# Optimization experiments

Hardware: AMD Instinct MI355X
Metric: run time of the kernel (lower is better)

## Reference

```python
import jax, jax.numpy as jnp
import numpy as np

B, N, K, D = 4096, 64, 48, 64   # batch, n_features, n_bins, d_embedding
F = N * D                        # flattened embedding dim
E, H, O = 8, 1024, 512           # experts, expert hidden, expert out
T, TH = 2, 256                   # tasks, tower hidden


def setup_inputs() -> dict:
    key = jax.random.key(0)
    ks = jax.random.split(key, 10)
    # PLE buffers from uniform bins linspace(0,1,K+1): w = 1/width, b = -edge/width
    edges = jnp.linspace(0.0, 1.0, K + 1)
    width = jnp.diff(edges)
    w = 1.0 / width                      # (K,)
    b = -edges[:-1] / width              # (K,)
    ple_weight = jnp.broadcast_to(w, (N, K)).astype(jnp.float32)
    ple_bias = jnp.broadcast_to(b, (N, K)).astype(jnp.float32)
    s = lambda fan_in: fan_in ** -0.5
    return {
        "x": jax.random.uniform(ks[0], (B, N), jnp.float32),
        "ple_weight": ple_weight,
        "ple_bias": ple_bias,
        "emb_W": jax.random.normal(ks[1], (N, K, D), jnp.float32) * s(K),
        "emb_b": jax.random.normal(ks[2], (N, D), jnp.float32) * s(K),
        "gate_W": jax.random.normal(ks[3], (F, E), jnp.float32) * s(F),
        "gate_b": jnp.zeros((E,), jnp.float32),
        "e_W1": jax.random.normal(ks[4], (E, F, H), jnp.float32) * s(F),
        "e_b1": jnp.zeros((E, H), jnp.float32),
        "e_W2": jax.random.normal(ks[5], (E, H, O), jnp.float32) * s(H),
        "e_b2": jnp.zeros((E, O), jnp.float32),
        "tw1": jax.random.normal(ks[6], (T, O, TH), jnp.float32) * s(O),
        "tb1": jnp.zeros((T, TH), jnp.float32),
        "tw2": jax.random.normal(ks[7], (T, TH, 1), jnp.float32) * s(TH),
        "tb2": jnp.zeros((T, 1), jnp.float32),
        "top_k": 2,
    }


def reference(x, ple_weight, ple_bias, emb_W, emb_b, gate_W, gate_b,
              e_W1, e_b1, e_W2, e_b2, tw1, tb1, tw2, tb2, top_k):
    # --- Piecewise Linear Encoding: (B, N) -> (B, N, K) ---
    enc = ple_bias + ple_weight * x[..., None]
    enc = jnp.concatenate([
        jnp.minimum(enc[..., :1], 1.0),
        jnp.clip(enc[..., 1:-1], 0.0, 1.0),
        jnp.maximum(enc[..., -1:], 0.0),
    ], axis=-1)
    # --- PLE embeddings via NLinear + ReLU: (B, N, K) -> (B, N, D) ---
    emb = jax.nn.relu(jnp.einsum("bnk,nkd->bnd", enc, emb_W) + emb_b)
    flat = emb.reshape(emb.shape[0], -1)                 # (B, F)
    # --- Sparse MoE gating (softmax + top-k renormalized) ---
    probs = jax.nn.softmax(flat @ gate_W + gate_b, axis=-1)   # (B, E)
    topv, topi = jax.lax.top_k(probs, top_k)
    topv = topv / jnp.sum(topv, axis=-1, keepdims=True)
    gates = jnp.zeros_like(probs).at[jnp.arange(probs.shape[0])[:, None], topi].set(topv)
    # --- Experts (computed densely, gated combine) ---
    h = jax.nn.relu(jnp.einsum("bf,efh->beh", flat, e_W1) + e_b1)   # (B, E, H)
    eo = jnp.einsum("beh,eho->beo", h, e_W2) + e_b2                 # (B, E, O)
    moe = jnp.einsum("be,beo->bo", gates, eo)                       # (B, O)
    # --- Task towers: per-task MLP -> scalar ---
    th = jax.nn.relu(jnp.einsum("bo,tos->bts", moe, tw1) + tb1)     # (B, T, TH)
    out = (jnp.einsum("bts,tsu->btu", th, tw2) + tb2)[..., 0]       # (B, T)
    return out
```

## Files before the change

kernel.cpp:

```cpp
#include <hip/hip_runtime.h>
#include <cstdint>

#define B_ 4096
#define N_ 64
#define K_ 48
#define D_ 64
#define F_ 4096
#define E_ 8
#define H_ 1024
#define O_ 512
#define T_ 2
#define TH_ 256
#define NSLOT (B_ * 2)

#define MAXT1 72

typedef float f32x4 __attribute__((ext_vector_type(4)));
typedef __bf16 bf16x8 __attribute__((ext_vector_type(8)));

__device__ __forceinline__ unsigned short f2bf(float f) {
    union { float f; unsigned int u; } v; v.f = f;
    unsigned int u = v.u;
    u += 0x7FFFu + ((u >> 16) & 1u);
    return (unsigned short)(u >> 16);
}

__device__ __forceinline__ void gload_lds16(const void* gptr, void* lptr) {
    auto* g = reinterpret_cast<const __attribute__((address_space(1))) unsigned int*>(
        reinterpret_cast<uintptr_t>(gptr));
    auto* l = reinterpret_cast<__attribute__((address_space(3))) unsigned int*>(
        reinterpret_cast<uintptr_t>(lptr));
    __builtin_amdgcn_global_load_lds(g, l, 16, 0, 0);
}

__global__ __launch_bounds__(64) void prefix_kernel(
    const float* __restrict__ embW, const float* __restrict__ embB,
    float* __restrict__ P)
{
    int n = blockIdx.x;
    int lane = threadIdx.x;
    float acc = embB[n * D_ + lane];
    const float* wsrc = embW + (size_t)n * K_ * D_ + lane;
    float* dst = P + (size_t)n * K_ * D_ + lane;
    #pragma unroll 8
    for (int k = 0; k < K_; ++k) {
        dst[k * D_] = acc;
        acc += wsrc[k * D_];
    }
}

__global__ __launch_bounds__(256) void ple_embed_kernel(
    const float* __restrict__ x, const float* __restrict__ plw,
    const float* __restrict__ plb, const float* __restrict__ embW,
    const float* __restrict__ P, const float* __restrict__ gateW,
    unsigned short* __restrict__ flat_bf, float* __restrict__ logits)
{
    __shared__ float gpart[4][E_];
    int b = blockIdx.x;
    int tid = threadIdx.x, lane = tid & 63, w = tid >> 6;

    float xl = x[b * N_ + lane];
    float gp[E_];
    #pragma unroll
    for (int e = 0; e < E_; ++e) gp[e] = 0.0f;

    #pragma unroll 4
    for (int i = 0; i < 16; ++i) {
        int n = w * 16 + i;
        float xn = __shfl(xl, n);
        const float* pw = plw + n * K_;
        const float* pb = plb + n * K_;
        float t = fmaf(pw[0], xn, pb[0]);
        int j = (int)t;
        j = max(0, min(K_ - 1, j));
        float f = fminf(fmaxf(fmaf(pw[j], xn, pb[j]), 0.0f), 1.0f);
        size_t base = ((size_t)n * K_ + j) * D_ + lane;
        float emb = fmaxf(fmaf(f, embW[base], P[base]), 0.0f);
        flat_bf[(size_t)b * F_ + n * D_ + lane] = f2bf(emb);

        const float4* gw4 = (const float4*)(gateW + (size_t)(n * D_ + lane) * E_);
        float4 g0 = gw4[0], g1 = gw4[1];
        gp[0] = fmaf(emb, g0.x, gp[0]);
        gp[1] = fmaf(emb, g0.y, gp[1]);
        gp[2] = fmaf(emb, g0.z, gp[2]);
        gp[3] = fmaf(emb, g0.w, gp[3]);
        gp[4] = fmaf(emb, g1.x, gp[4]);
        gp[5] = fmaf(emb, g1.y, gp[5]);
        gp[6] = fmaf(emb, g1.z, gp[6]);
        gp[7] = fmaf(emb, g1.w, gp[7]);
    }

    #pragma unroll
    for (int off = 32; off > 0; off >>= 1) {
        #pragma unroll
        for (int e = 0; e < E_; ++e) gp[e] += __shfl_down(gp[e], off);
    }
    if (lane == 0) {
        #pragma unroll
        for (int e = 0; e < E_; ++e) gpart[w][e] = gp[e];
    }
    __syncthreads();
    if (tid < E_)
        logits[b * E_ + tid] =
            gpart[0][tid] + gpart[1][tid] + gpart[2][tid] + gpart[3][tid];
}

__global__ __launch_bounds__(256) void gate_top2_kernel(
    const float* __restrict__ logits, const float* __restrict__ gate_b,
    int* __restrict__ topi, float* __restrict__ topg, int* __restrict__ counts)
{
    int b = blockIdx.x * 256 + threadIdx.x;
    int lane = threadIdx.x & 63;
    float l[E_];
    #pragma unroll
    for (int e = 0; e < E_; ++e) l[e] = logits[b * E_ + e] + gate_b[e];
    int e1 = 0; float v1 = l[0];
    #pragma unroll
    for (int e = 1; e < E_; ++e) if (l[e] > v1) { v1 = l[e]; e1 = e; }
    int e2 = -1; float v2 = -1e30f;
    #pragma unroll
    for (int e = 0; e < E_; ++e) if (e != e1 && l[e] > v2) { v2 = l[e]; e2 = e; }
    float ex = expf(v2 - v1);
    float g1 = 1.0f / (1.0f + ex);
    float g2 = ex / (1.0f + ex);
    topi[b * 2] = e1; topi[b * 2 + 1] = e2;
    topg[b * 2] = g1; topg[b * 2 + 1] = g2;
    #pragma unroll
    for (int e = 0; e < E_; ++e) {
        unsigned long long m1 = __ballot(e1 == e);
        unsigned long long m2 = __ballot(e2 == e);
        if (lane == 0) {
            int c = __popcll(m1) + __popcll(m2);
            if (c) atomicAdd(&counts[e], c);
        }
    }
}

__global__ void scan_kernel(const int* __restrict__ counts, int* __restrict__ offsets,
                            int* __restrict__ tiles1, int* __restrict__ ntiles) {
    int e = threadIdx.x;
    if (e >= E_) return;
    int c[E_];
    #pragma unroll
    for (int i = 0; i < E_; ++i) c[i] = counts[i];
    int off = 0, tb = 0, tot = 0, ttot = 0;
    #pragma unroll
    for (int i = 0; i < E_; ++i) {
        int t = (c[i] + 127) >> 7;
        if (i < e) { off += c[i]; tb += t; }
        tot += c[i]; ttot += t;
    }
    offsets[e] = off;
    if (e == 0) { offsets[E_] = tot; ntiles[0] = ttot; }
    int nt = (c[e] + 127) >> 7;
    for (int tr = 0; tr < nt; ++tr) tiles1[tb + tr] = (e << 16) | tr;
}

__global__ __launch_bounds__(256) void scatter_kernel(
    const int* __restrict__ topi, const float* __restrict__ topg,
    const int* __restrict__ offsets, int* __restrict__ cursors,
    int* __restrict__ rows, float* __restrict__ gatev)
{
    int b = blockIdx.x * 256 + threadIdx.x;
    int lane = threadIdx.x & 63;
    #pragma unroll
    for (int j = 0; j < 2; ++j) {
        int e = topi[b * 2 + j];
        float g = topg[b * 2 + j];
        #pragma unroll
        for (int ex = 0; ex < E_; ++ex) {
            unsigned long long m = __ballot(e == ex);
            if (e == ex) {
                int leader = __builtin_ctzll(m);
                int base = 0;
                if (lane == leader) base = atomicAdd(&cursors[ex], __popcll(m));
                base = __shfl(base, leader);
                int pos = base + __popcll(m & ((1ull << lane) - 1ull));
                int slot = offsets[ex] + pos;
                rows[slot] = b;
                gatev[slot] = g;
            }
        }
    }
}

__global__ __launch_bounds__(256) void transp_bf16_kernel(
    const float* __restrict__ in, unsigned short* __restrict__ out, int R, int C)
{
    __shared__ float tile[64][65];
    int ch = blockIdx.z;
    const float* src = in + (size_t)ch * R * C;
    unsigned short* dst = out + (size_t)ch * R * C;
    int c0 = blockIdx.x * 64, r0 = blockIdx.y * 64;
    int lane = threadIdx.x & 63, w = threadIdx.x >> 6;
    #pragma unroll
    for (int i = 0; i < 16; ++i) {
        int r = w * 16 + i;
        tile[r][lane] = src[(size_t)(r0 + r) * C + c0 + lane];
    }
    __syncthreads();
    #pragma unroll
    for (int i = 0; i < 16; ++i) {
        int c = w * 16 + i;
        dst[(size_t)(c0 + c) * R + r0 + lane] = f2bf(tile[lane][c]);
    }
}

__global__ __launch_bounds__(256) void fc1_kernel(
    const unsigned short* __restrict__ Abf,
    const unsigned short* __restrict__ Wbt,
    const float* __restrict__ bias,
    const int* __restrict__ rows, const int* __restrict__ offsets,
    const int* __restrict__ tiles1, const int* __restrict__ ntiles,
    unsigned short* __restrict__ Hbf)
{
    int bid = blockIdx.x;
    int tile = bid >> 3, cn = bid & 7;
    if (tile >= ntiles[0]) return;
    int te = tiles1[tile];
    int e = te >> 16, tr = te & 0xffff;
    int m0 = offsets[e], mEnd = offsets[e + 1];
    int Me = mEnd - m0;

    __shared__ alignas(16) unsigned short As[128 * 64];
    __shared__ alignas(16) unsigned short Bs[128 * 64];

    int tid = threadIdx.x, lane = tid & 63, wv = tid >> 6;
    int lr = lane >> 3;
    int pchunk = lane & 7;
    int cg = pchunk ^ lr;

    const unsigned short* aptr[4];
    const unsigned short* bptr[4];
    #pragma unroll
    for (int i = 0; i < 4; ++i) {
        int reg = wv * 4 + i;
        int rowA = reg * 8 + lr;
        int slot = min(m0 + tr * 128 + rowA, mEnd - 1);
        aptr[i] = Abf + (size_t)rows[slot] * F_ + cg * 8;
        int rowB = cn * 128 + reg * 8 + lr;
        bptr[i] = Wbt + ((size_t)e * H_ + rowB) * (size_t)F_ + cg * 8;
    }

    f32x4 zero = {0.f, 0.f, 0.f, 0.f};
    f32x4 acc[4][4];
    #pragma unroll
    for (int i = 0; i < 4; ++i)
        #pragma unroll
        for (int j = 0; j < 4; ++j) acc[i][j] = zero;

    int wvM = wv >> 1, wvN = wv & 1;
    int m16 = lane & 15, q = lane >> 4;

    for (int k0 = 0; k0 < F_; k0 += 64) {
        __syncthreads();
        #pragma unroll
        for (int i = 0; i < 4; ++i) {
            int reg = wv * 4 + i;
            gload_lds16(aptr[i] + k0, &As[reg * 512]);
            gload_lds16(bptr[i] + k0, &Bs[reg * 512]);
        }
        __syncthreads();
        #pragma unroll
        for (int ks = 0; ks < 2; ++ks) {
            bf16x8 af[4], bfg[4];
            #pragma unroll
            for (int mt = 0; mt < 4; ++mt) {
                int m = wvM * 64 + mt * 16 + m16;
                int pos = (ks * 4 + q) ^ (m & 7);
                af[mt] = *(const bf16x8*)&As[m * 64 + pos * 8];
            }
            #pragma unroll
            for (int nt = 0; nt < 4; ++nt) {
                int n = wvN * 64 + nt * 16 + m16;
                int pos = (ks * 4 + q) ^ (n & 7);
                bfg[nt] = *(const bf16x8*)&Bs[n * 64 + pos * 8];
            }
            #pragma unroll
            for (int mt = 0; mt < 4; ++mt)
                #pragma unroll
                for (int nt = 0; nt < 4; ++nt)
                    acc[mt][nt] = __builtin_amdgcn_mfma_f32_16x16x32_bf16(
                        af[mt], bfg[nt], acc[mt][nt], 0, 0, 0);
        }
    }

    #pragma unroll
    for (int nt = 0; nt < 4; ++nt) {
        int col = cn * 128 + wvN * 64 + nt * 16 + m16;
        float bv = bias[e * H_ + col];
        #pragma unroll
        for (int mt = 0; mt < 4; ++mt) {
            int rbase = tr * 128 + wvM * 64 + mt * 16 + q * 4;
            #pragma unroll
            for (int r = 0; r < 4; ++r) {
                int rr = rbase + r;
                if (rr < Me) {
                    float v = fmaxf(acc[mt][nt][r] + bv, 0.0f);
                    Hbf[(size_t)(m0 + rr) * H_ + col] = f2bf(v);
                }
            }
        }
    }
}

__global__ __launch_bounds__(256) void fc2_kernel(
    const unsigned short* __restrict__ Hbf,
    const unsigned short* __restrict__ Wbt,
    const float* __restrict__ bias,
    const int* __restrict__ rows, const float* __restrict__ gatev,
    const int* __restrict__ offsets, const int* __restrict__ tiles1,
    const int* __restrict__ ntiles, float* __restrict__ moe)
{
    int bid = blockIdx.x;
    int tile = bid >> 3, cn = bid & 7;
    if (tile >= ntiles[0]) return;
    int te = tiles1[tile];
    int e = te >> 16, tr = te & 0xffff;
    int m0 = offsets[e], mEnd = offsets[e + 1];
    int Me = mEnd - m0;

    __shared__ alignas(16) unsigned short As[128 * 64];
    __shared__ alignas(16) unsigned short Bs[64 * 64];

    int tid = threadIdx.x, lane = tid & 63, wv = tid >> 6;
    int lr = lane >> 3;
    int pchunk = lane & 7;
    int cg = pchunk ^ lr;

    const unsigned short* aptr[4];
    const unsigned short* bptr[2];
    #pragma unroll
    for (int i = 0; i < 4; ++i) {
        int rowA = (wv * 4 + i) * 8 + lr;
        int slot = min(m0 + tr * 128 + rowA, mEnd - 1);
        aptr[i] = Hbf + (size_t)slot * H_ + cg * 8;
    }
    #pragma unroll
    for (int i = 0; i < 2; ++i) {
        int rowB = cn * 64 + (wv * 2 + i) * 8 + lr;
        bptr[i] = Wbt + ((size_t)e * O_ + rowB) * (size_t)H_ + cg * 8;
    }

    f32x4 zero = {0.f, 0.f, 0.f, 0.f};
    f32x4 acc[4][2];
    #pragma unroll
    for (int i = 0; i < 4; ++i)
        #pragma unroll
        for (int j = 0; j < 2; ++j) acc[i][j] = zero;

    int wvM = wv >> 1, wvN = wv & 1;
    int m16 = lane & 15, q = lane >> 4;

    for (int k0 = 0; k0 < H_; k0 += 64) {
        __syncthreads();
        #pragma unroll
        for (int i = 0; i < 4; ++i)
            gload_lds16(aptr[i] + k0, &As[(wv * 4 + i) * 512]);
        #pragma unroll
        for (int i = 0; i < 2; ++i)
            gload_lds16(bptr[i] + k0, &Bs[(wv * 2 + i) * 512]);
        __syncthreads();
        #pragma unroll
        for (int ks = 0; ks < 2; ++ks) {
            bf16x8 af[4], bfg[2];
            #pragma unroll
            for (int mt = 0; mt < 4; ++mt) {
                int m = wvM * 64 + mt * 16 + m16;
                int pos = (ks * 4 + q) ^ (m & 7);
                af[mt] = *(const bf16x8*)&As[m * 64 + pos * 8];
            }
            #pragma unroll
            for (int nt = 0; nt < 2; ++nt) {
                int n = wvN * 32 + nt * 16 + m16;
                int pos = (ks * 4 + q) ^ (n & 7);
                bfg[nt] = *(const bf16x8*)&Bs[n * 64 + pos * 8];
            }
            #pragma unroll
            for (int mt = 0; mt < 4; ++mt)
                #pragma unroll
                for (int nt = 0; nt < 2; ++nt)
                    acc[mt][nt] = __builtin_amdgcn_mfma_f32_16x16x32_bf16(
                        af[mt], bfg[nt], acc[mt][nt], 0, 0, 0);
        }
    }

    #pragma unroll
    for (int nt = 0; nt < 2; ++nt) {
        int col = cn * 64 + wvN * 32 + nt * 16 + m16;
        float bv = bias[e * O_ + col];
        #pragma unroll
        for (int mt = 0; mt < 4; ++mt) {
            int rbase = tr * 128 + wvM * 64 + mt * 16 + q * 4;
            #pragma unroll
            for (int r = 0; r < 4; ++r) {
                int rr = rbase + r;
                if (rr < Me) {
                    int slot = m0 + rr;
                    float g = gatev[slot];
                    int b = rows[slot];
                    atomicAdd(&moe[(size_t)b * O_ + col], g * (acc[mt][nt][r] + bv));
                }
            }
        }
    }
}

__global__ __launch_bounds__(256) void tower_kernel(
    const float* __restrict__ moe, const float* __restrict__ tw1,
    const float* __restrict__ tb1, const float* __restrict__ tw2,
    const float* __restrict__ tb2, float* __restrict__ out)
{
    __shared__ float ms[8 * O_];
    __shared__ float red[16][4];
    int b0 = blockIdx.x * 8;
    int tid = threadIdx.x, lane = tid & 63, wv = tid >> 6;
    for (int idx = tid; idx < 8 * O_; idx += 256)
        ms[idx] = moe[(size_t)b0 * O_ + idx];
    __syncthreads();

    int s = tid;
    float a0[8], a1[8];
    float bv0 = tb1[s], bv1 = tb1[TH_ + s];
    #pragma unroll
    for (int i = 0; i < 8; ++i) { a0[i] = bv0; a1[i] = bv1; }

    for (int o = 0; o < O_; o += 4) {
        float w0[4], w1[4];
        #pragma unroll
        for (int u = 0; u < 4; ++u) {
            w0[u] = tw1[(size_t)(o + u) * TH_ + s];
            w1[u] = tw1[(size_t)(O_ + o + u) * TH_ + s];
        }
        #pragma unroll
        for (int i = 0; i < 8; ++i) {
            float4 mv = *(const float4*)&ms[i * O_ + o];
            a0[i] = fmaf(mv.x, w0[0], a0[i]);
            a0[i] = fmaf(mv.y, w0[1], a0[i]);
            a0[i] = fmaf(mv.z, w0[2], a0[i]);
            a0[i] = fmaf(mv.w, w0[3], a0[i]);
            a1[i] = fmaf(mv.x, w1[0], a1[i]);
            a1[i] = fmaf(mv.y, w1[1], a1[i]);
            a1[i] = fmaf(mv.z, w1[2], a1[i]);
            a1[i] = fmaf(mv.w, w1[3], a1[i]);
        }
    }

    float w2a = tw2[s], w2b = tw2[TH_ + s];
    #pragma unroll
    for (int i = 0; i < 8; ++i) {
        float p0 = fmaxf(a0[i], 0.0f) * w2a;
        float p1 = fmaxf(a1[i], 0.0f) * w2b;
        #pragma unroll
        for (int off = 32; off > 0; off >>= 1) {
            p0 += __shfl_down(p0, off);
            p1 += __shfl_down(p1, off);
        }
        if (lane == 0) { red[i * 2 + 0][wv] = p0; red[i * 2 + 1][wv] = p1; }
    }
    __syncthreads();
    if (tid < 16) {
        int i = tid >> 1, t = tid & 1;
        float v = red[tid][0] + red[tid][1] + red[tid][2] + red[tid][3] + tb2[t];
        out[(size_t)(b0 + i) * T_ + t] = v;
    }
}

extern "C" void kernel_launch(void* const* d_in, const int* in_sizes, int n_in,
                              void* d_out, int out_size, void* d_ws, size_t ws_size,
                              hipStream_t stream)
{
    const float* x     = (const float*)d_in[0];
    const float* plw   = (const float*)d_in[1];
    const float* plb   = (const float*)d_in[2];
    const float* embW  = (const float*)d_in[3];
    const float* embB  = (const float*)d_in[4];
    const float* gateW = (const float*)d_in[5];
    const float* gateB = (const float*)d_in[6];
    const float* eW1   = (const float*)d_in[7];
    const float* eB1   = (const float*)d_in[8];
    const float* eW2   = (const float*)d_in[9];
    const float* eB2   = (const float*)d_in[10];
    const float* tw1   = (const float*)d_in[11];
    const float* tb1   = (const float*)d_in[12];
    const float* tw2   = (const float*)d_in[13];
    const float* tb2   = (const float*)d_in[14];
    float* out = (float*)d_out;

    char* w = (char*)d_ws;
    auto alloc = [&](size_t bytes) {
        char* p = w; w += (bytes + 255) & ~(size_t)255; return p;
    };
    unsigned short* flat_bf = (unsigned short*)alloc((size_t)B_ * F_ * 2);
    unsigned short* W1bt    = (unsigned short*)alloc((size_t)E_ * H_ * F_ * 2);
    unsigned short* W2bt    = (unsigned short*)alloc((size_t)E_ * O_ * H_ * 2);
    unsigned short* Hbf     = (unsigned short*)alloc((size_t)NSLOT * H_ * 2);
    float* Ppre    = (float*)alloc((size_t)N_ * K_ * D_ * 4);
    float* logits  = (float*)alloc((size_t)B_ * E_ * 4);
    float* moe     = (float*)alloc((size_t)B_ * O_ * 4);
    int*   topi    = (int*)alloc((size_t)B_ * 2 * 4);
    float* topg    = (float*)alloc((size_t)B_ * 2 * 4);
    int*   rows    = (int*)alloc((size_t)NSLOT * 4);
    float* gatev   = (float*)alloc((size_t)NSLOT * 4);
    int*   counts  = (int*)alloc(E_ * 4);
    int*   offsets = (int*)alloc((E_ + 1) * 4);
    int*   cursors = (int*)alloc(E_ * 4);
    int*   tiles1  = (int*)alloc(MAXT1 * 4);
    int*   ntiles  = (int*)alloc(2 * 4);

    hipMemsetAsync(moe, 0, (size_t)B_ * O_ * 4, stream);
    hipMemsetAsync(counts, 0, E_ * 4, stream);
    hipMemsetAsync(cursors, 0, E_ * 4, stream);

    prefix_kernel<<<N_, 64, 0, stream>>>(embW, embB, Ppre);
    ple_embed_kernel<<<B_, 256, 0, stream>>>(x, plw, plb, embW, Ppre, gateW,
                                             flat_bf, logits);
    transp_bf16_kernel<<<dim3(H_ / 64, F_ / 64, E_), 256, 0, stream>>>(eW1, W1bt, F_, H_);
    transp_bf16_kernel<<<dim3(O_ / 64, H_ / 64, E_), 256, 0, stream>>>(eW2, W2bt, H_, O_);
    gate_top2_kernel<<<B_ / 256, 256, 0, stream>>>(logits, gateB, topi, topg, counts);
    scan_kernel<<<1, 64, 0, stream>>>(counts, offsets, tiles1, ntiles);
    scatter_kernel<<<B_ / 256, 256, 0, stream>>>(topi, topg, offsets, cursors, rows, gatev);
    fc1_kernel<<<MAXT1 * 8, 256, 0, stream>>>(flat_bf, W1bt, eB1, rows, offsets,
                                              tiles1, ntiles, Hbf);
    fc2_kernel<<<MAXT1 * 8, 256, 0, stream>>>(Hbf, W2bt, eB2, rows, gatev, offsets,
                                              tiles1, ntiles, moe);
    tower_kernel<<<B_ / 8, 256, 0, stream>>>(moe, tw1, tb1, tw2, tb2, out);
}
```

Before: 574.8 us.

## Pre-swizzle expert weights into MFMA fragment layout and load B directly to registers

The weight conversion kernel now writes bf16 expert weights in a per-16x32 MFMA fragment order, so each lane can load its B operand with one contiguous 16-byte global read. Staging B through LDS is dropped in fc1 and fc2. fc1 tiles shrink from 128 to 64 columns with twice as many blocks, which raises parallelism but re-reads each A tile across 16 column blocks. B loads now go straight from global memory into registers with no LDS reuse across waves, so each wave's B fetch latency sits exposed inside the k-loop.

```diff
diff --git a/kernel.cpp b/kernel.cpp
--- a/kernel.cpp
+++ b/kernel.cpp
@@ -184,35 +184,145 @@
     }
 }
 
-__global__ __launch_bounds__(256) void transp_bf16_kernel(
+__global__ __launch_bounds__(256) void wfrag_kernel(
     const float* __restrict__ in, unsigned short* __restrict__ out, int R, int C)
 {
     __shared__ float tile[64][65];
-    int ch = blockIdx.z;
-    const float* src = in + (size_t)ch * R * C;
-    unsigned short* dst = out + (size_t)ch * R * C;
-    int c0 = blockIdx.x * 64, r0 = blockIdx.y * 64;
+    int e = blockIdx.z;
+    int rb = blockIdx.x, cb = blockIdx.y;
+    const float* src = in + (size_t)e * R * C + (size_t)(rb * 64) * C + cb * 64;
     int lane = threadIdx.x & 63, w = threadIdx.x >> 6;
     #pragma unroll
     for (int i = 0; i < 16; ++i) {
         int r = w * 16 + i;
-        tile[r][lane] = src[(size_t)(r0 + r) * C + c0 + lane];
+        tile[r][lane] = src[(size_t)r * C + lane];
     }
     __syncthreads();
-    #pragma unroll
-    for (int i = 0; i < 16; ++i) {
-        int c = w * 16 + i;
-        dst[(size_t)(c0 + c) * R + r0 + lane] = f2bf(tile[lane][c]);
+    int NB = C >> 4, KB = R >> 5;
+    #pragma unroll
+    for (int it = 0; it < 2; ++it) {
+        int t = threadIdx.x + it * 256;
+        int n0r = t >> 7, k0r = (t >> 6) & 1, ln = t & 63;
+        int q = ln >> 4, nl = ln & 15;
+        unsigned short v[8];
+        #pragma unroll
+        for (int j = 0; j < 8; ++j)
+            v[j] = f2bf(tile[k0r * 32 + q * 8 + j][n0r * 16 + nl]);
+        size_t didx = (((size_t)e * NB + cb * 4 + n0r) * KB + rb * 2 + k0r) * 512
+                      + (size_t)ln * 8;
+        uint4 pk;
+        pk.x = v[0] | ((unsigned)v[1] << 16);
+        pk.y = v[2] | ((unsigned)v[3] << 16);
+        pk.z = v[4] | ((unsigned)v[5] << 16);
+        pk.w = v[6] | ((unsigned)v[7] << 16);
+        *(uint4*)&out[didx] = pk;
     }
 }
 
 __global__ __launch_bounds__(256) void fc1_kernel(
     const unsigned short* __restrict__ Abf,
-    const unsigned short* __restrict__ Wbt,
+    const unsigned short* __restrict__ Wf,
     const float* __restrict__ bias,
     const int* __restrict__ rows, const int* __restrict__ offsets,
     const int* __restrict__ tiles1, const int* __restrict__ ntiles,
     unsigned short* __restrict__ Hbf)
+{
+    int bid = blockIdx.x;
+    int tile = bid >> 4, cn = bid & 15;
+    if (tile >= ntiles[0]) return;
+    int te = tiles1[tile];
+    int e = te >> 16, tr = te & 0xffff;
+    int m0 = offsets[e], mEnd = offsets[e + 1];
+    int Me = mEnd - m0;
+
+    __shared__ alignas(16) unsigned short As[128 * 64];
+
+    int tid = threadIdx.x, lane = tid & 63, wv = tid >> 6;
+    int lr = lane >> 3;
+    int cg = (lane & 7) ^ lr;
+
+    const unsigned short* aptr[4];
+    #pragma unroll
+    for (int i = 0; i < 4; ++i) {
+        int rowA = (wv * 4 + i) * 8 + lr;
+        int slot = min(m0 + tr * 128 + rowA, mEnd - 1);
+        aptr[i] = Abf + (size_t)rows[slot] * F_ + cg * 8;
+    }
+
+    int wvM = wv >> 1, wvN = wv & 1;
+    int m16 = lane & 15, q = lane >> 4;
+
+    const unsigned short* bbase[2];
+    #pragma unroll
+    for (int nt = 0; nt < 2; ++nt) {
+        int n0 = cn * 4 + wvN * 2 + nt;
+        bbase[nt] = Wf + (((size_t)e * (H_ / 16) + n0) * (F_ / 32)) * 512
+                    + (size_t)lane * 8;
+    }
+
+    f32x4 zero = {0.f, 0.f, 0.f, 0.f};
+    f32x4 acc[4][2];
+    #pragma unroll
+    for (int i = 0; i < 4; ++i)
+        #pragma unroll
+        for (int j = 0; j < 2; ++j) acc[i][j] = zero;
+
+    for (int k0 = 0; k0 < F_; k0 += 64) {
+        __syncthreads();
+        #pragma unroll
+        for (int i = 0; i < 4; ++i)
+            gload_lds16(aptr[i] + k0, &As[(wv * 4 + i) * 512]);
+        bf16x8 bfr[2][2];
+        #pragma unroll
+        for (int nt = 0; nt < 2; ++nt)
+            #pragma unroll
+            for (int ks = 0; ks < 2; ++ks)
+                bfr[nt][ks] = *(const bf16x8*)(bbase[nt] + (size_t)k0 * 16 + ks * 512);
+        __syncthreads();
+        #pragma unroll
+        for (int ks = 0; ks < 2; ++ks) {
+            bf16x8 af[4];
+            #pragma unroll
+            for (int mt = 0; mt < 4; ++mt) {
+                int m = wvM * 64 + mt * 16 + m16;
+                int pos = (ks * 4 + q) ^ (m & 7);
+                af[mt] = *(const bf16x8*)&As[m * 64 + pos * 8];
+            }
+            #pragma unroll
+            for (int mt = 0; mt < 4; ++mt)
+                #pragma unroll
+                for (int nt = 0; nt < 2; ++nt)
+                    acc[mt][nt] = __builtin_amdgcn_mfma_f32_16x16x32_bf16(
+                        af[mt], bfr[nt][ks], acc[mt][nt], 0, 0, 0);
+        }
+    }
+
+    #pragma unroll
+    for (int nt = 0; nt < 2; ++nt) {
+        int col = cn * 64 + wvN * 32 + nt * 16 + m16;
+        float bv = bias[e * H_ + col];
+        #pragma unroll
+        for (int mt = 0; mt < 4; ++mt) {
+            int rbase = tr * 128 + wvM * 64 + mt * 16 + q * 4;
+            #pragma unroll
+            for (int r = 0; r < 4; ++r) {
+                int rr = rbase + r;
+                if (rr < Me) {
+                    float v = fmaxf(acc[mt][nt][r] + bv, 0.0f);
+                    Hbf[(size_t)(m0 + rr) * H_ + col] = f2bf(v);
+                }
+            }
+        }
+    }
+}
+
+__global__ __launch_bounds__(256) void fc2_kernel(
+    const unsigned short* __restrict__ Hbf,
+    const unsigned short* __restrict__ Wf,
+    const float* __restrict__ bias,
+    const int* __restrict__ rows, const float* __restrict__ gatev,
+    const int* __restrict__ offsets, const int* __restrict__ tiles1,
+    const int* __restrict__ ntiles, float* __restrict__ moe)
 {
     int bid = blockIdx.x;
     int tile = bid >> 3, cn = bid & 7;
@@ -223,47 +333,52 @@
     int Me = mEnd - m0;
 
     __shared__ alignas(16) unsigned short As[128 * 64];
-    __shared__ alignas(16) unsigned short Bs[128 * 64];
 
     int tid = threadIdx.x, lane = tid & 63, wv = tid >> 6;
     int lr = lane >> 3;
-    int pchunk = lane & 7;
-    int cg = pchunk ^ lr;
+    int cg = (lane & 7) ^ lr;
 
     const unsigned short* aptr[4];
-    const unsigned short* bptr[4];
     #pragma unroll
     for (int i = 0; i < 4; ++i) {
-        int reg = wv * 4 + i;
-        int rowA = reg * 8 + lr;
+        int rowA = (wv * 4 + i) * 8 + lr;
         int slot = min(m0 + tr * 128 + rowA, mEnd - 1);
-        aptr[i] = Abf + (size_t)rows[slot] * F_ + cg * 8;
-        int rowB = cn * 128 + reg * 8 + lr;
-        bptr[i] = Wbt + ((size_t)e * H_ + rowB) * (size_t)F_ + cg * 8;
-    }
-
-    f32x4 zero = {0.f, 0.f, 0.f, 0.f};
-    f32x4 acc[4][4];
-    #pragma unroll
-    for (int i = 0; i < 4; ++i)
-        #pragma unroll
-        for (int j = 0; j < 4; ++j) acc[i][j] = zero;
+        aptr[i] = Hbf + (size_t)slot * H_ + cg * 8;
+    }
 
     int wvM = wv >> 1, wvN = wv & 1;
     int m16 = lane & 15, q = lane >> 4;
 
-    for (int k0 = 0; k0 < F_; k0 += 64) {
+    const unsigned short* bbase[2];
+    #pragma unroll
+    for (int nt = 0; nt < 2; ++nt) {
+        int n0 = cn * 4 + wvN * 2 + nt;
+        bbase[nt] = Wf + (((size_t)e * (O_ / 16) + n0) * (H_ / 32)) * 512
+                    + (size_t)lane * 8;
+    }
+
+    f32x4 zero = {0.f, 0.f, 0.f, 0.f};
+    f32x4 acc[4][2];
+    #pragma unroll
+    for (int i = 0; i < 4; ++i)
+        #pragma unroll
+        for (int j = 0; j < 2; ++j) acc[i][j] = zero;
+
+    for (int k0 = 0; k0 < H_; k0 += 64) {
         __syncthreads();
         #pragma unroll
-        for (int i = 0; i < 4; ++i) {
-            int reg = wv * 4 + i;
-            gload_lds16(aptr[i] + k0, &As[reg * 512]);
-            gload_lds16(bptr[i] + k0, &Bs[reg * 512]);
-        }
+        for (int i = 0; i < 4; ++i)
+            gload_lds16(aptr[i] + k0, &As[(wv * 4 + i) * 512]);
+        bf16x8 bfr[2][2];
+        #pragma unroll
+        for (int nt = 0; nt < 2; ++nt)
+            #pragma unroll
+            for (int ks = 0; ks < 2; ++ks)
+                bfr[nt][ks] = *(const bf16x8*)(bbase[nt] + (size_t)k0 * 16 + ks * 512);
         __syncthreads();
         #pragma unroll
         for (int ks = 0; ks < 2; ++ks) {
-            bf16x8 af[4], bfg[4];
+            bf16x8 af[4];
             #pragma unroll
             for (int mt = 0; mt < 4; ++mt) {
                 int m = wvM * 64 + mt * 16 + m16;
@@ -271,117 +386,11 @@
                 af[mt] = *(const bf16x8*)&As[m * 64 + pos * 8];
             }
             #pragma unroll
-            for (int nt = 0; nt < 4; ++nt) {
-                int n = wvN * 64 + nt * 16 + m16;
-                int pos = (ks * 4 + q) ^ (n & 7);
-                bfg[nt] = *(const bf16x8*)&Bs[n * 64 + pos * 8];
-            }
-            #pragma unroll
-            for (int mt = 0; mt < 4; ++mt)
-                #pragma unroll
-                for (int nt = 0; nt < 4; ++nt)
-                    acc[mt][nt] = __builtin_amdgcn_mfma_f32_16x16x32_bf16(
-                        af[mt], bfg[nt], acc[mt][nt], 0, 0, 0);
-        }
-    }
-
-    #pragma unroll
-    for (int nt = 0; nt < 4; ++nt) {
-        int col = cn * 128 + wvN * 64 + nt * 16 + m16;
-        float bv = bias[e * H_ + col];
-        #pragma unroll
-        for (int mt = 0; mt < 4; ++mt) {
-            int rbase = tr * 128 + wvM * 64 + mt * 16 + q * 4;
-            #pragma unroll
-            for (int r = 0; r < 4; ++r) {
-                int rr = rbase + r;
-                if (rr < Me) {
-                    float v = fmaxf(acc[mt][nt][r] + bv, 0.0f);
-                    Hbf[(size_t)(m0 + rr) * H_ + col] = f2bf(v);
-                }
-            }
-        }
-    }
-}
-
-__global__ __launch_bounds__(256) void fc2_kernel(
-    const unsigned short* __restrict__ Hbf,
-    const unsigned short* __restrict__ Wbt,
-    const float* __restrict__ bias,
-    const int* __restrict__ rows, const float* __restrict__ gatev,
-    const int* __restrict__ offsets, const int* __restrict__ tiles1,
-    const int* __restrict__ ntiles, float* __restrict__ moe)
-{
-    int bid = blockIdx.x;
-    int tile = bid >> 3, cn = bid & 7;
-    if (tile >= ntiles[0]) return;
-    int te = tiles1[tile];
-    int e = te >> 16, tr = te & 0xffff;
-    int m0 = offsets[e], mEnd = offsets[e + 1];
-    int Me = mEnd - m0;
-
-    __shared__ alignas(16) unsigned short As[128 * 64];
-    __shared__ alignas(16) unsigned short Bs[64 * 64];
-
-    int tid = threadIdx.x, lane = tid & 63, wv = tid >> 6;
-    int lr = lane >> 3;
-    int pchunk = lane & 7;
-    int cg = pchunk ^ lr;
-
-    const unsigned short* aptr[4];
-    const unsigned short* bptr[2];
-    #pragma unroll
-    for (int i = 0; i < 4; ++i) {
-        int rowA = (wv * 4 + i) * 8 + lr;
-        int slot = min(m0 + tr * 128 + rowA, mEnd - 1);
-        aptr[i] = Hbf + (size_t)slot * H_ + cg * 8;
-    }
-    #pragma unroll
-    for (int i = 0; i < 2; ++i) {
-        int rowB = cn * 64 + (wv * 2 + i) * 8 + lr;
-        bptr[i] = Wbt + ((size_t)e * O_ + rowB) * (size_t)H_ + cg * 8;
-    }
-
-    f32x4 zero = {0.f, 0.f, 0.f, 0.f};
-    f32x4 acc[4][2];
-    #pragma unroll
-    for (int i = 0; i < 4; ++i)
-        #pragma unroll
-        for (int j = 0; j < 2; ++j) acc[i][j] = zero;
-
-    int wvM = wv >> 1, wvN = wv & 1;
-    int m16 = lane & 15, q = lane >> 4;
-
-    for (int k0 = 0; k0 < H_; k0 += 64) {
-        __syncthreads();
-        #pragma unroll
-        for (int i = 0; i < 4; ++i)
-            gload_lds16(aptr[i] + k0, &As[(wv * 4 + i) * 512]);
-        #pragma unroll
-        for (int i = 0; i < 2; ++i)
-            gload_lds16(bptr[i] + k0, &Bs[(wv * 2 + i) * 512]);
-        __syncthreads();
-        #pragma unroll
-        for (int ks = 0; ks < 2; ++ks) {
-            bf16x8 af[4], bfg[2];
-            #pragma unroll
-            for (int mt = 0; mt < 4; ++mt) {
-                int m = wvM * 64 + mt * 16 + m16;
-                int pos = (ks * 4 + q) ^ (m & 7);
-                af[mt] = *(const bf16x8*)&As[m * 64 + pos * 8];
-            }
-            #pragma unroll
-            for (int nt = 0; nt < 2; ++nt) {
-                int n = wvN * 32 + nt * 16 + m16;
-                int pos = (ks * 4 + q) ^ (n & 7);
-                bfg[nt] = *(const bf16x8*)&Bs[n * 64 + pos * 8];
-            }
-            #pragma unroll
             for (int mt = 0; mt < 4; ++mt)
                 #pragma unroll
                 for (int nt = 0; nt < 2; ++nt)
                     acc[mt][nt] = __builtin_amdgcn_mfma_f32_16x16x32_bf16(
-                        af[mt], bfg[nt], acc[mt][nt], 0, 0, 0);
+                        af[mt], bfr[nt][ks], acc[mt][nt], 0, 0, 0);
         }
     }
 
@@ -492,8 +501,8 @@
         char* p = w; w += (bytes + 255) & ~(size_t)255; return p;
     };
     unsigned short* flat_bf = (unsigned short*)alloc((size_t)B_ * F_ * 2);
-    unsigned short* W1bt    = (unsigned short*)alloc((size_t)E_ * H_ * F_ * 2);
-    unsigned short* W2bt    = (unsigned short*)alloc((size_t)E_ * O_ * H_ * 2);
+    unsigned short* W1f     = (unsigned short*)alloc((size_t)E_ * H_ * F_ * 2);
+    unsigned short* W2f     = (unsigned short*)alloc((size_t)E_ * O_ * H_ * 2);
     unsigned short* Hbf     = (unsigned short*)alloc((size_t)NSLOT * H_ * 2);
     float* Ppre    = (float*)alloc((size_t)N_ * K_ * D_ * 4);
     float* logits  = (float*)alloc((size_t)B_ * E_ * 4);
@@ -515,14 +524,14 @@
     prefix_kernel<<<N_, 64, 0, stream>>>(embW, embB, Ppre);
     ple_embed_kernel<<<B_, 256, 0, stream>>>(x, plw, plb, embW, Ppre, gateW,
                                              flat_bf, logits);
-    transp_bf16_kernel<<<dim3(H_ / 64, F_ / 64, E_), 256, 0, stream>>>(eW1, W1bt, F_, H_);
-    transp_bf16_kernel<<<dim3(O_ / 64, H_ / 64, E_), 256, 0, stream>>>(eW2, W2bt, H_, O_);
+    wfrag_kernel<<<dim3(F_ / 64, H_ / 64, E_), 256, 0, stream>>>(eW1, W1f, F_, H_);
+    wfrag_kernel<<<dim3(H_ / 64, O_ / 64, E_), 256, 0, stream>>>(eW2, W2f, H_, O_);
     gate_top2_kernel<<<B_ / 256, 256, 0, stream>>>(logits, gateB, topi, topg, counts);
     scan_kernel<<<1, 64, 0, stream>>>(counts, offsets, tiles1, ntiles);
     scatter_kernel<<<B_ / 256, 256, 0, stream>>>(topi, topg, offsets, cursors, rows, gatev);
-    fc1_kernel<<<MAXT1 * 8, 256, 0, stream>>>(flat_bf, W1bt, eB1, rows, offsets,
-                                              tiles1, ntiles, Hbf);
-    fc2_kernel<<<MAXT1 * 8, 256, 0, stream>>>(Hbf, W2bt, eB2, rows, gatev, offsets,
+    fc1_kernel<<<MAXT1 * 16, 256, 0, stream>>>(flat_bf, W1f, eB1, rows, offsets,
+                                               tiles1, ntiles, Hbf);
+    fc2_kernel<<<MAXT1 * 8, 256, 0, stream>>>(Hbf, W2f, eB2, rows, gatev, offsets,
                                               tiles1, ntiles, moe);
     tower_kernel<<<B_ / 8, 256, 0, stream>>>(moe, tw1, tb1, tw2, tb2, out);
 }
```

New measurement: 558.2 us. 1.03x faster.
